# Performance work log

Hardware: AMD Instinct MI355X
Metric: run time of the kernel (lower is better)

## Reference

```python
import jax, jax.numpy as jnp
import numpy as np

NEG_BIG = -9e15  # matches torch -9000000000000000.0

def setup_inputs() -> dict:
    key = jax.random.key(0)
    k1, k2, k3, k4 = jax.random.split(key, 4)
    B, N, F_IN, F_OUT = 8, 2048, 128, 64
    x = jax.random.normal(k1, (B, N, F_IN), dtype=jnp.float32)
    adj = jax.random.randint(k2, (B, N, N), 0, 2, dtype=jnp.int32)
    # xavier_uniform-style init for params
    limW = float(np.sqrt(6.0 / (F_IN + F_OUT)))
    W = jax.random.uniform(k3, (F_IN, F_OUT), minval=-limW, maxval=limW, dtype=jnp.float32)
    lima = float(np.sqrt(6.0 / (2 * F_OUT + 1)))
    a = jax.random.uniform(k4, (2 * F_OUT, 1), minval=-lima, maxval=lima, dtype=jnp.float32)
    return {"x": x, "adj": adj, "W": W, "a": a}

def reference(x, adj, W, a):
    # x: [B, N, F_in], adj: [B, N, N], W: [F_in, F_out], a: [2*F_out, 1]
    h = jnp.einsum('bnf,fo->bno', x, W)            # [B, N, F_out]
    F_out = W.shape[1]
    # The repeat/cat construction computes a_input[b,i,j] = [h_i ; h_j], so
    # a_input @ a decomposes into f1_i + f2_j without the O(N^2 * 2F) tensor.
    f1 = h @ a[:F_out, 0]                          # [B, N]
    f2 = h @ a[F_out:, 0]                          # [B, N]
    e = jnp.tanh(f1[:, :, None] + f2[:, None, :])  # [B, N, N]
    att = jnp.where(adj > 0, e, NEG_BIG)
    att = jax.nn.softmax(att, axis=2)              # [B, N, N]
    h_prime = jnp.einsum('bmn,bno->bmo', att, h)   # [B, N, F_out]
    return jax.nn.elu(h_prime)                     # concat=True branch
```

## Files before the change

### kernel.cpp

```cpp
#include <hip/hip_runtime.h>
#include <math.h>

#define BB 8
#define NN 2048
#define FIN 128
#define FOUT 64
#define TI 16
#define TJ 512
#define TJP (TJ + 8)
#define NTILE (NN / TJ)

typedef short bf16x8 __attribute__((ext_vector_type(8)));
typedef float f32x4 __attribute__((ext_vector_type(4)));

__device__ __forceinline__ float exp_tanh(float z) {
    float zc = fminf(fmaxf(z, -15.f), 15.f);
    float u = __expf(zc + zc);
    float tn = (u - 1.f) * __builtin_amdgcn_rcpf(u + 1.f);
    return __expf(tn);
}

__device__ __forceinline__ unsigned short f2bf(float x) {
    union { float f; unsigned u; } v; v.f = x;
    unsigned r = v.u + 0x7FFF + ((v.u >> 16) & 1);
    return (unsigned short)(r >> 16);
}

__global__ __launch_bounds__(256, 2) void gat_k1(const float* __restrict__ x,
                                                 const float* __restrict__ W,
                                                 const float* __restrict__ a,
                                                 unsigned short* __restrict__ ht,
                                                 float* __restrict__ f1,
                                                 float* __restrict__ f2) {
    __shared__ __attribute__((aligned(16))) float Wl[FIN][FOUT];
    __shared__ __attribute__((aligned(16))) float xs[16][FIN];
    int t = threadIdx.x;

    const float4* W4 = (const float4*)W;
    float4* Wl4 = (float4*)&Wl[0][0];
#pragma unroll
    for (int kk = 0; kk < 8; ++kk) Wl4[t + 256 * kk] = W4[t + 256 * kk];

    size_t row0 = (size_t)blockIdx.x * 16;
    const float4* x4 = (const float4*)(x + row0 * FIN);
    float4* xs4 = (float4*)&xs[0][0];
#pragma unroll
    for (int kk = 0; kk < 2; ++kk) xs4[t + 256 * kk] = x4[t + 256 * kk];
    __syncthreads();

    int c = t & 63;
    int rq = t >> 6;
    float acc[4] = {0.f, 0.f, 0.f, 0.f};
#pragma unroll 8
    for (int k = 0; k < FIN; ++k) {
        float wv = Wl[k][c];
        acc[0] = fmaf(xs[rq][k], wv, acc[0]);
        acc[1] = fmaf(xs[rq + 4][k], wv, acc[1]);
        acc[2] = fmaf(xs[rq + 8][k], wv, acc[2]);
        acc[3] = fmaf(xs[rq + 12][k], wv, acc[3]);
    }
    float a1c = a[c], a2c = a[FOUT + c];
#pragma unroll
    for (int m = 0; m < 4; ++m) {
        size_t bn = row0 + rq + 4 * m;
        int b = (int)(bn >> 11);
        int n = (int)(bn & 2047);
        ht[((size_t)b * FOUT + c) * NN + n] = f2bf(acc[m]);
        float p1 = acc[m] * a1c;
        float p2 = acc[m] * a2c;
#pragma unroll
        for (int off = 32; off > 0; off >>= 1) {
            p1 += __shfl_down(p1, off, 64);
            p2 += __shfl_down(p2, off, 64);
        }
        if (c == 0) { f1[bn] = p1; f2[bn] = p2; }
    }
}

__global__ __launch_bounds__(256, 4) void gat_k2(const int* __restrict__ adj,
                                                 const unsigned short* __restrict__ ht,
                                                 const float* __restrict__ f1,
                                                 const float* __restrict__ f2,
                                                 float* __restrict__ accg,
                                                 float* __restrict__ rs) {
    __shared__ __attribute__((aligned(16))) unsigned short pb[TI][TJP];
    __shared__ __attribute__((aligned(16))) float f2s[TJ];
    __shared__ float f1s[TI];

    int t = threadIdx.x;
    int i0 = blockIdx.x * TI;
    int j0 = blockIdx.y * TJ;
    int b = blockIdx.z;

    int lane = t & 63;
    int w = t >> 6;
    int mrow = lane & 15;
    int quad = lane >> 4;

    int j4 = t & 127;
    int r0 = t >> 7;

    const int* adjbase = adj + (((size_t)b * NN + i0) * NN) + j0 + 4 * j4;
    int4 avreg[8];
#pragma unroll
    for (int kk = 0; kk < 8; ++kk)
        avreg[kk] = *(const int4*)(adjbase + (size_t)(r0 + 2 * kk) * NN);

    ((float2*)f2s)[t] = ((const float2*)(f2 + (size_t)b * NN + j0))[t];
    if (t < TI) f1s[t] = f1[(size_t)b * NN + i0 + t];
    __syncthreads();

    float f1r[8];
#pragma unroll
    for (int kk = 0; kk < 8; ++kk) f1r[kk] = f1s[r0 + 2 * kk];

    float4 fv = ((const float4*)f2s)[j4];
    float ps[8];
#pragma unroll
    for (int kk = 0; kk < 8; ++kk) {
        int4 av = avreg[kk];
        float f1i = f1r[kk];
        float4 p;
        p.x = (av.x > 0) ? exp_tanh(f1i + fv.x) : 0.f;
        p.y = (av.y > 0) ? exp_tanh(f1i + fv.y) : 0.f;
        p.z = (av.z > 0) ? exp_tanh(f1i + fv.z) : 0.f;
        p.w = (av.w > 0) ? exp_tanh(f1i + fv.w) : 0.f;
        ps[kk] = p.x + p.y + p.z + p.w;
        ushort4 pk;
        pk.x = f2bf(p.x); pk.y = f2bf(p.y);
        pk.z = f2bf(p.z); pk.w = f2bf(p.w);
        *(ushort4*)&pb[r0 + 2 * kk][4 * j4] = pk;
    }
    __syncthreads();

    const unsigned short* hp =
        ht + ((size_t)b * FOUT + w * 16 + mrow) * NN + j0 + 8 * quad;
    const unsigned short* prow = &pb[mrow][8 * quad];
    f32x4 acc = {0.f, 0.f, 0.f, 0.f};
#pragma unroll 4
    for (int ch = 0; ch < TJ / 32; ++ch) {
        bf16x8 af = *(const bf16x8*)(prow + 32 * ch);
        bf16x8 bf = *(const bf16x8*)(hp + 32 * ch);
        acc = __builtin_amdgcn_mfma_f32_16x16x32_bf16(af, bf, acc, 0, 0, 0);
    }

#pragma unroll
    for (int kk = 0; kk < 8; ++kk) {
        float s = ps[kk];
#pragma unroll
        for (int off = 32; off > 0; off >>= 1) s += __shfl_down(s, off, 64);
        if (lane == 0)
            atomicAdd(&rs[(size_t)b * NN + i0 + r0 + 2 * kk], s);
    }
    float* ap = accg + ((size_t)b * NN + i0) * FOUT + w * 16 + mrow;
#pragma unroll
    for (int u = 0; u < 4; ++u) {
        int row = quad * 4 + u;
        atomicAdd(&ap[(size_t)row * FOUT], acc[u]);
    }
}

__global__ __launch_bounds__(256) void gat_k3(const float* __restrict__ accg,
                                              const float* __restrict__ rs,
                                              float* __restrict__ out) {
    int g4 = blockIdx.x * 256 + threadIdx.x;
    int row = g4 >> 4;
    float rinv = __builtin_amdgcn_rcpf(rs[row]);
    float4 v = ((const float4*)accg)[g4];
    float4 o;
    float sx = v.x * rinv; o.x = (sx > 0.f) ? sx : expm1f(sx);
    float sy = v.y * rinv; o.y = (sy > 0.f) ? sy : expm1f(sy);
    float sz = v.z * rinv; o.z = (sz > 0.f) ? sz : expm1f(sz);
    float sw = v.w * rinv; o.w = (sw > 0.f) ? sw : expm1f(sw);
    ((float4*)out)[g4] = o;
}

extern "C" void kernel_launch(void* const* d_in, const int* in_sizes, int n_in,
                              void* d_out, int out_size, void* d_ws, size_t ws_size,
                              hipStream_t stream) {
    const float* x   = (const float*)d_in[0];
    const int*   adj = (const int*)d_in[1];
    const float* W   = (const float*)d_in[2];
    const float* a   = (const float*)d_in[3];
    float* out = (float*)d_out;

    unsigned short* ht = (unsigned short*)d_ws;
    float* f1   = (float*)(ht + (size_t)BB * FOUT * NN);
    float* f2   = f1 + (size_t)BB * NN;
    float* accg = f2 + (size_t)BB * NN;
    float* rs   = accg + (size_t)BB * NN * FOUT;
    hipMemsetAsync(accg, 0, ((size_t)BB * NN * FOUT + (size_t)BB * NN) * 4, stream);

    gat_k1<<<dim3(BB * NN / 16), dim3(256), 0, stream>>>(x, W, a, ht, f1, f2);
    gat_k2<<<dim3(NN / TI, NTILE, BB), dim3(256), 0, stream>>>(adj, ht, f1, f2, accg, rs);
    gat_k3<<<dim3(BB * NN * FOUT / 1024), dim3(256), 0, stream>>>(accg, rs, out);
}
```

Baseline: 233.2 us.

## Pre-pack adjacency into bitmasks and replace atomics with per-tile partial buffers

The first kernel gains extra blocks that read the int32 adjacency matrix and pack it into 32-bit masks. The attention kernel then reads those masks instead of int4 loads, which cuts its memory traffic and register pressure. The atomic accumulation of the output and row sums is replaced by plain stores into per-tile partial buffers, and the final kernel adds those partials. This also removes the memset, at the cost of larger workspace and an extra reduction read in the last kernel.

```diff
diff --git a/kernel.cpp b/kernel.cpp
--- a/kernel.cpp
+++ b/kernel.cpp
@@ -9,6 +9,7 @@
 #define TJ 512
 #define TJP (TJ + 8)
 #define NTILE (NN / TJ)
+#define PACKB 4096
 
 typedef short bf16x8 __attribute__((ext_vector_type(8)));
 typedef float f32x4 __attribute__((ext_vector_type(4)));
@@ -26,22 +27,40 @@
     return (unsigned short)(r >> 16);
 }
 
-__global__ __launch_bounds__(256, 2) void gat_k1(const float* __restrict__ x,
-                                                 const float* __restrict__ W,
-                                                 const float* __restrict__ a,
-                                                 unsigned short* __restrict__ ht,
-                                                 float* __restrict__ f1,
-                                                 float* __restrict__ f2) {
+__global__ __launch_bounds__(256, 2) void gat_k01(const float* __restrict__ x,
+                                                  const int* __restrict__ adj,
+                                                  const float* __restrict__ W,
+                                                  const float* __restrict__ a,
+                                                  unsigned short* __restrict__ ht,
+                                                  float* __restrict__ f1,
+                                                  float* __restrict__ f2,
+                                                  unsigned* __restrict__ pm) {
     __shared__ __attribute__((aligned(16))) float Wl[FIN][FOUT];
     __shared__ __attribute__((aligned(16))) float xs[16][FIN];
     int t = threadIdx.x;
 
+    if (blockIdx.x < PACKB) {
+        size_t g = (size_t)blockIdx.x * 256 + t;
+        const int4* src = (const int4*)(adj + (g << 5));
+        unsigned m = 0;
+#pragma unroll
+        for (int q = 0; q < 8; ++q) {
+            int4 v = src[q];
+            m |= (v.x > 0 ? 1u : 0u) << (4 * q);
+            m |= (v.y > 0 ? 2u : 0u) << (4 * q);
+            m |= (v.z > 0 ? 4u : 0u) << (4 * q);
+            m |= (v.w > 0 ? 8u : 0u) << (4 * q);
+        }
+        pm[g] = m;
+        return;
+    }
+
     const float4* W4 = (const float4*)W;
     float4* Wl4 = (float4*)&Wl[0][0];
 #pragma unroll
     for (int kk = 0; kk < 8; ++kk) Wl4[t + 256 * kk] = W4[t + 256 * kk];
 
-    size_t row0 = (size_t)blockIdx.x * 16;
+    size_t row0 = (size_t)(blockIdx.x - PACKB) * 16;
     const float4* x4 = (const float4*)(x + row0 * FIN);
     float4* xs4 = (float4*)&xs[0][0];
 #pragma unroll
@@ -77,19 +96,20 @@
     }
 }
 
-__global__ __launch_bounds__(256, 4) void gat_k2(const int* __restrict__ adj,
+__global__ __launch_bounds__(256, 4) void gat_k2(const unsigned* __restrict__ pm,
                                                  const unsigned short* __restrict__ ht,
                                                  const float* __restrict__ f1,
                                                  const float* __restrict__ f2,
                                                  float* __restrict__ accg,
-                                                 float* __restrict__ rs) {
+                                                 float* __restrict__ rsp) {
     __shared__ __attribute__((aligned(16))) unsigned short pb[TI][TJP];
     __shared__ __attribute__((aligned(16))) float f2s[TJ];
     __shared__ float f1s[TI];
 
     int t = threadIdx.x;
     int i0 = blockIdx.x * TI;
-    int j0 = blockIdx.y * TJ;
+    int jt = blockIdx.y;
+    int j0 = jt * TJ;
     int b = blockIdx.z;
 
     int lane = t & 63;
@@ -100,11 +120,11 @@
     int j4 = t & 127;
     int r0 = t >> 7;
 
-    const int* adjbase = adj + (((size_t)b * NN + i0) * NN) + j0 + 4 * j4;
-    int4 avreg[8];
+    const unsigned* pmb = pm + (((size_t)b * NN + i0) << 6) + (j0 >> 5) + (j4 >> 3);
+    unsigned mreg[8];
 #pragma unroll
     for (int kk = 0; kk < 8; ++kk)
-        avreg[kk] = *(const int4*)(adjbase + (size_t)(r0 + 2 * kk) * NN);
+        mreg[kk] = pmb[(size_t)(r0 + 2 * kk) << 6];
 
     ((float2*)f2s)[t] = ((const float2*)(f2 + (size_t)b * NN + j0))[t];
     if (t < TI) f1s[t] = f1[(size_t)b * NN + i0 + t];
@@ -115,16 +135,17 @@
     for (int kk = 0; kk < 8; ++kk) f1r[kk] = f1s[r0 + 2 * kk];
 
     float4 fv = ((const float4*)f2s)[j4];
+    int sh = 4 * (j4 & 7);
     float ps[8];
 #pragma unroll
     for (int kk = 0; kk < 8; ++kk) {
-        int4 av = avreg[kk];
+        unsigned nib = mreg[kk] >> sh;
         float f1i = f1r[kk];
         float4 p;
-        p.x = (av.x > 0) ? exp_tanh(f1i + fv.x) : 0.f;
-        p.y = (av.y > 0) ? exp_tanh(f1i + fv.y) : 0.f;
-        p.z = (av.z > 0) ? exp_tanh(f1i + fv.z) : 0.f;
-        p.w = (av.w > 0) ? exp_tanh(f1i + fv.w) : 0.f;
+        p.x = (nib & 1u) ? exp_tanh(f1i + fv.x) : 0.f;
+        p.y = (nib & 2u) ? exp_tanh(f1i + fv.y) : 0.f;
+        p.z = (nib & 4u) ? exp_tanh(f1i + fv.z) : 0.f;
+        p.w = (nib & 8u) ? exp_tanh(f1i + fv.w) : 0.f;
         ps[kk] = p.x + p.y + p.z + p.w;
         ushort4 pk;
         pk.x = f2bf(p.x); pk.y = f2bf(p.y);
@@ -150,23 +171,31 @@
 #pragma unroll
         for (int off = 32; off > 0; off >>= 1) s += __shfl_down(s, off, 64);
         if (lane == 0)
-            atomicAdd(&rs[(size_t)b * NN + i0 + r0 + 2 * kk], s);
-    }
-    float* ap = accg + ((size_t)b * NN + i0) * FOUT + w * 16 + mrow;
-#pragma unroll
-    for (int u = 0; u < 4; ++u) {
-        int row = quad * 4 + u;
-        atomicAdd(&ap[(size_t)row * FOUT], acc[u]);
-    }
+            rsp[(size_t)(jt * 2 + (w & 1)) * (BB * NN) +
+                (size_t)b * NN + i0 + r0 + 2 * kk] = s;
+    }
+    float* ap = accg + (((size_t)jt * BB + b) * NN + i0) * FOUT + w * 16 + mrow;
+#pragma unroll
+    for (int u = 0; u < 4; ++u)
+        ap[(size_t)(quad * 4 + u) * FOUT] = acc[u];
 }
 
 __global__ __launch_bounds__(256) void gat_k3(const float* __restrict__ accg,
-                                              const float* __restrict__ rs,
+                                              const float* __restrict__ rsp,
                                               float* __restrict__ out) {
     int g4 = blockIdx.x * 256 + threadIdx.x;
     int row = g4 >> 4;
-    float rinv = __builtin_amdgcn_rcpf(rs[row]);
-    float4 v = ((const float4*)accg)[g4];
+    float s = 0.f;
+#pragma unroll
+    for (int q = 0; q < 2 * NTILE; ++q) s += rsp[(size_t)q * (BB * NN) + row];
+    float rinv = __builtin_amdgcn_rcpf(s);
+    const float4* ag = (const float4*)accg;
+    float4 v = ag[g4];
+#pragma unroll
+    for (int tl = 1; tl < NTILE; ++tl) {
+        float4 u = ag[(size_t)tl * (BB * NN * FOUT / 4) + g4];
+        v.x += u.x; v.y += u.y; v.z += u.z; v.w += u.w;
+    }
     float4 o;
     float sx = v.x * rinv; o.x = (sx > 0.f) ? sx : expm1f(sx);
     float sy = v.y * rinv; o.y = (sy > 0.f) ? sy : expm1f(sy);
@@ -187,11 +216,13 @@
     unsigned short* ht = (unsigned short*)d_ws;
     float* f1   = (float*)(ht + (size_t)BB * FOUT * NN);
     float* f2   = f1 + (size_t)BB * NN;
-    float* accg = f2 + (size_t)BB * NN;
-    float* rs   = accg + (size_t)BB * NN * FOUT;
-    hipMemsetAsync(accg, 0, ((size_t)BB * NN * FOUT + (size_t)BB * NN) * 4, stream);
-
-    gat_k1<<<dim3(BB * NN / 16), dim3(256), 0, stream>>>(x, W, a, ht, f1, f2);
-    gat_k2<<<dim3(NN / TI, NTILE, BB), dim3(256), 0, stream>>>(adj, ht, f1, f2, accg, rs);
-    gat_k3<<<dim3(BB * NN * FOUT / 1024), dim3(256), 0, stream>>>(accg, rs, out);
-}
+    unsigned* pm = (unsigned*)(f2 + (size_t)BB * NN);
+    float* accg = (float*)(pm + (size_t)BB * NN * (NN / 32));
+    float* rsp  = accg + (size_t)NTILE * BB * NN * FOUT;
+
+    gat_k01<<<dim3(PACKB + BB * NN / 16), dim3(256), 0, stream>>>(
+        x, adj, W, a, ht, f1, f2, pm);
+    gat_k2<<<dim3(NN / TI, NTILE, BB), dim3(256), 0, stream>>>(
+        pm, ht, f1, f2, accg, rsp);
+    gat_k3<<<dim3(BB * NN * FOUT / 1024), dim3(256), 0, stream>>>(accg, rsp, out);
+}
```

Measured after the change: 249.9 us. +7.2%, slower.
